# Kernel optimization log

Measured on AMD Instinct MI355X. Metric: run time of the kernel, lower is better.

The kernel has to match this reference:

```python
import jax, jax.numpy as jnp
import numpy as np

N, BIT, NUM_CLASSES = 512, 64, 100
ALPHA = 5.0   # config['alpha']
LAM = 1.0     # config['lambda']


def setup_inputs() -> dict:
    key = jax.random.key(0)
    k_u, k_lbl = jax.random.split(key)
    u = jax.random.normal(k_u, (N, BIT), dtype=jnp.float32)
    labels = jax.random.randint(k_lbl, (N,), 0, NUM_CLASSES)
    y = jax.nn.one_hot(labels, NUM_CLASSES, dtype=jnp.float32)  # [N, C]
    return {"u": u, "y": y}


def reference(u, y):
    dt = u.dtype
    ip = u @ u.T                       # [N, N] inner products
    s = (y @ y.T) > 0                  # [N, N] similarity mask (bool)
    pos = s.astype(dt)                 # positive-pair mask per row
    neg = 1.0 - pos                    # negative-pair mask per row
    npos = pos.sum(axis=1)             # [N]
    nneg = neg.sum(axis=1)             # [N]
    valid = (npos > 0) & (nneg > 0)    # rows contributing to loss1

    # triple[r, p, n] = ip[r, p] - ip[r, n] - alpha, clamped as in the original
    triple = jnp.clip(ip[:, :, None] - ip[:, None, :] - ALPHA, -100.0, 50.0)  # [N, N, N]
    # per-element loss: -(t - log(1 + exp(t)))  (clamp keeps exp finite)
    f = jnp.log1p(jnp.exp(triple)) - triple

    w = pos[:, :, None] * neg[:, None, :]            # valid (pos, neg) pair mask
    pair_count = jnp.maximum(npos * nneg, 1.0)       # avoid div-by-zero on skipped rows
    row_loss = (f * w).sum(axis=(1, 2)) / pair_count  # masked mean per row

    count = valid.sum().astype(dt)
    loss1 = jnp.where(count > 0,
                      jnp.where(valid, row_loss, 0.0).sum() / jnp.maximum(count, 1.0),
                      jnp.asarray(0.0, dt))
    loss2 = LAM * jnp.mean((u - jnp.sign(u)) ** 2)   # quantization penalty
    return loss1 + loss2
```

## Files before the change

### kernel.cpp

```cpp
#include <hip/hip_runtime.h>
#include <hip/hip_bf16.h>
#include <math.h>

#define N 512
#define BIT 64
#define NUM_CLASSES 100
#define ALPHA 5.0f
#define LAM 1.0f

__global__ void prep_kernel(const float* __restrict__ u,
                            const float* __restrict__ y,
                            int* __restrict__ labels,
                            float* __restrict__ acc) {
    int tid = threadIdx.x;
    if (tid < 4) acc[tid] = 0.0f;

    int lbl = 0;
    const float* yr = y + (size_t)tid * NUM_CLASSES;
    for (int c = 0; c < NUM_CLASSES; ++c) {
        if (yr[c] > 0.5f) lbl = c;
    }
    labels[tid] = lbl;

    float s = 0.0f;
    const float* ur = u + (size_t)tid * BIT;
    for (int k = 0; k < BIT; ++k) {
        float v = ur[k];
        float sg = (v > 0.0f) ? 1.0f : ((v < 0.0f) ? -1.0f : 0.0f);
        float d = v - sg;
        s += d * d;
    }
    for (int off = 32; off > 0; off >>= 1) s += __shfl_down(s, off, 64);
    __syncthreads();
    if ((tid & 63) == 0) atomicAdd(&acc[2], s);
}

__global__ void ip_kernel(const float* __restrict__ u, float* __restrict__ ip) {
    __shared__ float As[16][BIT + 1];
    __shared__ float Bs[16][BIT + 1];
    int bx = blockIdx.x, by = blockIdx.y;
    int tx = threadIdx.x, ty = threadIdx.y;
    int tid = ty * 16 + tx;

    for (int e = tid; e < 16 * BIT; e += 256) {
        int r = e >> 6;
        int c = e & 63;
        As[r][c] = u[((size_t)(by * 16 + r)) * BIT + c];
        Bs[r][c] = u[((size_t)(bx * 16 + r)) * BIT + c];
    }
    __syncthreads();

    float accv = 0.0f;
    #pragma unroll
    for (int k = 0; k < BIT; ++k) accv += As[ty][k] * Bs[tx][k];
    ip[((size_t)(by * 16 + ty)) * N + (bx * 16 + tx)] = accv;
}

__global__ void row_kernel(const float* __restrict__ ip,
                           const int* __restrict__ labels,
                           float* __restrict__ acc) {
    int r = blockIdx.x;
    int tid = threadIdx.x;

    __shared__ float d[N];
    __shared__ int   lab[N];
    __shared__ int   poslist[N];
    __shared__ int   npos_s;
    __shared__ float wsum[4];

    if (tid == 0) npos_s = 0;
    for (int i = tid; i < N; i += 256) {
        d[i]   = ip[(size_t)r * N + i];
        lab[i] = labels[i];
    }
    __syncthreads();

    int lr = lab[r];
    for (int i = tid; i < N; i += 256) {
        if (lab[i] == lr) {
            int idx = atomicAdd(&npos_s, 1);
            poslist[idx] = i;
        }
    }
    __syncthreads();

    int npos = npos_s;
    int nneg = N - npos;

    float fsum = 0.0f;
    for (int pi = 0; pi < npos; ++pi) {
        float dp = d[poslist[pi]];
        for (int n = tid; n < N; n += 256) {
            if (lab[n] != lr) {
                float t = dp - d[n] - ALPHA;
                t = fminf(fmaxf(t, -100.0f), 50.0f);
                float f = (t > 0.0f) ? log1pf(expf(-t))
                                     : (log1pf(expf(t)) - t);
                fsum += f;
            }
        }
    }

    for (int off = 32; off > 0; off >>= 1) fsum += __shfl_down(fsum, off, 64);
    if ((tid & 63) == 0) wsum[tid >> 6] = fsum;
    __syncthreads();

    if (tid == 0) {
        float total = wsum[0] + wsum[1] + wsum[2] + wsum[3];
        bool valid = (npos > 0) && (nneg > 0);
        float pair_count = fmaxf((float)npos * (float)nneg, 1.0f);
        float row_loss = total / pair_count;
        if (valid) {
            atomicAdd(&acc[0], row_loss);
            atomicAdd(&acc[1], 1.0f);
        }
    }
}

__global__ void finish_kernel(const float* __restrict__ acc,
                              float* __restrict__ out) {
    float count = acc[1];
    float loss1 = (count > 0.0f) ? (acc[0] / fmaxf(count, 1.0f)) : 0.0f;
    float loss2 = LAM * acc[2] / (float)(N * BIT);
    out[0] = loss1 + loss2;
}

extern "C" void kernel_launch(void* const* d_in, const int* in_sizes, int n_in,
                              void* d_out, int out_size, void* d_ws, size_t ws_size,
                              hipStream_t stream) {
    const float* u = (const float*)d_in[0];
    const float* y = (const float*)d_in[1];
    float* out = (float*)d_out;

    char* ws = (char*)d_ws;
    float* ip     = (float*)ws;
    int*   labels = (int*)(ws + (size_t)N * N * sizeof(float));
    float* acc    = (float*)(ws + (size_t)N * N * sizeof(float)
                                + (size_t)N * sizeof(int));

    prep_kernel<<<1, 512, 0, stream>>>(u, y, labels, acc);

    dim3 gb(N / 16, N / 16), tb(16, 16);
    ip_kernel<<<gb, tb, 0, stream>>>(u, ip);

    row_kernel<<<N, 256, 0, stream>>>(ip, labels, acc);

    finish_kernel<<<1, 1, 0, stream>>>(acc, out);
}
```

Baseline: 92.40 us.

## Fuse inner-product, quantization and finish into row kernel with last-block reduction

```diff
diff --git a/kernel.cpp b/kernel.cpp
--- a/kernel.cpp
+++ b/kernel.cpp
@@ -8,60 +8,27 @@
 #define ALPHA 5.0f
 #define LAM 1.0f
 
-__global__ void prep_kernel(const float* __restrict__ u,
-                            const float* __restrict__ y,
-                            int* __restrict__ labels,
-                            float* __restrict__ acc) {
-    int tid = threadIdx.x;
-    if (tid < 4) acc[tid] = 0.0f;
 
+__global__ void label_kernel(const float* __restrict__ y,
+                             int* __restrict__ labels) {
+    int r = blockIdx.x * 64 + threadIdx.x;
+    const float* yr = y + (size_t)r * NUM_CLASSES;
     int lbl = 0;
-    const float* yr = y + (size_t)tid * NUM_CLASSES;
     for (int c = 0; c < NUM_CLASSES; ++c) {
         if (yr[c] > 0.5f) lbl = c;
     }
-    labels[tid] = lbl;
-
-    float s = 0.0f;
-    const float* ur = u + (size_t)tid * BIT;
-    for (int k = 0; k < BIT; ++k) {
-        float v = ur[k];
-        float sg = (v > 0.0f) ? 1.0f : ((v < 0.0f) ? -1.0f : 0.0f);
-        float d = v - sg;
-        s += d * d;
-    }
-    for (int off = 32; off > 0; off >>= 1) s += __shfl_down(s, off, 64);
-    __syncthreads();
-    if ((tid & 63) == 0) atomicAdd(&acc[2], s);
+    labels[r] = lbl;
 }
 
-__global__ void ip_kernel(const float* __restrict__ u, float* __restrict__ ip) {
-    __shared__ float As[16][BIT + 1];
-    __shared__ float Bs[16][BIT + 1];
-    int bx = blockIdx.x, by = blockIdx.y;
-    int tx = threadIdx.x, ty = threadIdx.y;
-    int tid = ty * 16 + tx;
-
-    for (int e = tid; e < 16 * BIT; e += 256) {
-        int r = e >> 6;
-        int c = e & 63;
-        As[r][c] = u[((size_t)(by * 16 + r)) * BIT + c];
-        Bs[r][c] = u[((size_t)(bx * 16 + r)) * BIT + c];
-    }
-    __syncthreads();
-
-    float accv = 0.0f;
-    #pragma unroll
-    for (int k = 0; k < BIT; ++k) accv += As[ty][k] * Bs[tx][k];
-    ip[((size_t)(by * 16 + ty)) * N + (bx * 16 + tx)] = accv;
-}
-
-__global__ void row_kernel(const float* __restrict__ ip,
-                           const int* __restrict__ labels,
-                           float* __restrict__ acc) {
+__global__ void fused_kernel(const float* __restrict__ u,
+                             const int* __restrict__ labels,
+                             float* __restrict__ acc,
+                             int* __restrict__ ctr,
+                             float* __restrict__ out) {
     int r = blockIdx.x;
     int tid = threadIdx.x;
 
+    __shared__ float ur[BIT];
     __shared__ float d[N];
     __shared__ int   lab[N];
     __shared__ int   poslist[N];
@@ -69,9 +36,34 @@
     __shared__ float wsum[4];
 
     if (tid == 0) npos_s = 0;
-    for (int i = tid; i < N; i += 256) {
-        d[i]   = ip[(size_t)r * N + i];
-        lab[i] = labels[i];
+    if (tid < BIT) ur[tid] = u[(size_t)r * BIT + tid];
+    for (int i = tid; i < N; i += 256) lab[i] = labels[i];
+    __syncthreads();
+
+    float4 urv[16];
+    const float4* urf = (const float4*)ur;
+    #pragma unroll
+    for (int k = 0; k < 16; ++k) urv[k] = urf[k];
+
+    for (int n = tid; n < N; n += 256) {
+        const float4* un = (const float4*)(u + (size_t)n * BIT);
+        float s = 0.0f;
+        #pragma unroll
+        for (int k = 0; k < 16; ++k) {
+            float4 a = un[k];
+            float4 b = urv[k];
+            s += a.x * b.x + a.y * b.y + a.z * b.z + a.w * b.w;
+        }
+        d[n] = s;
+    }
+
+    if (tid < 64) {
+        float v = ur[tid];
+        float sg = (v > 0.0f) ? 1.0f : ((v < 0.0f) ? -1.0f : 0.0f);
+        float dd = v - sg;
+        float s2 = dd * dd;
+        for (int off = 32; off > 0; off >>= 1) s2 += __shfl_down(s2, off, 64);
+        if (tid == 0) atomicAdd(&acc[2], s2);
     }
     __syncthreads();
 
@@ -109,20 +101,20 @@
         float total = wsum[0] + wsum[1] + wsum[2] + wsum[3];
         bool valid = (npos > 0) && (nneg > 0);
         float pair_count = fmaxf((float)npos * (float)nneg, 1.0f);
-        float row_loss = total / pair_count;
         if (valid) {
-            atomicAdd(&acc[0], row_loss);
+            atomicAdd(&acc[0], total / pair_count);
             atomicAdd(&acc[1], 1.0f);
         }
+        __threadfence();
+        int done = atomicAdd(ctr, 1);
+        if (done == N - 1) {
+            float s1  = atomicAdd(&acc[0], 0.0f);
+            float cnt = atomicAdd(&acc[1], 0.0f);
+            float s2  = atomicAdd(&acc[2], 0.0f);
+            float loss1 = (cnt > 0.0f) ? (s1 / fmaxf(cnt, 1.0f)) : 0.0f;
+            out[0] = loss1 + LAM * s2 / (float)(N * BIT);
+        }
     }
-}
-
-__global__ void finish_kernel(const float* __restrict__ acc,
-                              float* __restrict__ out) {
-    float count = acc[1];
-    float loss1 = (count > 0.0f) ? (acc[0] / fmaxf(count, 1.0f)) : 0.0f;
-    float loss2 = LAM * acc[2] / (float)(N * BIT);
-    out[0] = loss1 + loss2;
 }
 
 extern "C" void kernel_launch(void* const* d_in, const int* in_sizes, int n_in,
@@ -133,17 +125,12 @@
     float* out = (float*)d_out;
 
     char* ws = (char*)d_ws;
-    float* ip     = (float*)ws;
-    int*   labels = (int*)(ws + (size_t)N * N * sizeof(float));
-    float* acc    = (float*)(ws + (size_t)N * N * sizeof(float)
-                                + (size_t)N * sizeof(int));
+    float* acc    = (float*)ws;
+    int*   ctr    = (int*)(ws + 12);
+    int*   labels = (int*)(ws + 64);
 
-    prep_kernel<<<1, 512, 0, stream>>>(u, y, labels, acc);
+    hipMemsetAsync(ws, 0, 64, stream);
 
-    dim3 gb(N / 16, N / 16), tb(16, 16);
-    ip_kernel<<<gb, tb, 0, stream>>>(u, ip);
-
-    row_kernel<<<N, 256, 0, stream>>>(ip, labels, acc);
-
-    finish_kernel<<<1, 1, 0, stream>>>(acc, out);
+    label_kernel<<<8, 64, 0, stream>>>(y, labels);
+    fused_kernel<<<N, 256, 0, stream>>>(u, labels, acc, ctr, out);
 }
```

New measurement: 93.05 us. About the same (+0.7%).
